# Optimization experiments

Measured on AMD Instinct MI355X. Metric: run time of the kernel, lower is better.

Reference implementation:

```python
import jax, jax.numpy as jnp
import numpy as np

H = 256        # hidden_size
NC = 15        # num_components (decode steps)
V = 26         # vocab_size
E = 64         # embed_dim
B = 65536      # batch


def setup_inputs() -> dict:
    key = jax.random.key(0)
    ks = jax.random.split(key, 8)
    return {
        "context": jax.random.normal(ks[0], (B, H), jnp.float32),
        "embed_table": (jax.random.normal(ks[1], (V, E), jnp.float32) * 0.02),
        "start_embed": (jax.random.normal(ks[2], (E,), jnp.float32) * 0.02),
        "Wp": jax.random.normal(ks[3], (H, H), jnp.float32) / np.sqrt(H),
        "bp": jnp.zeros((H,), jnp.float32),
        "Wi": jax.random.normal(ks[4], (H + E, 4 * H), jnp.float32) / np.sqrt(H + E),
        "Wh": jax.random.normal(ks[5], (H, 4 * H), jnp.float32) / np.sqrt(H),
        "bh": jnp.zeros((4 * H,), jnp.float32),
        "Wo": jax.random.normal(ks[6], (H, V), jnp.float32) / np.sqrt(H),
        "bo": jnp.zeros((V,), jnp.float32),
        "seed": 0,
    }


def _lstm_step(c, h, x, Wi, Wh, bh):
    # flax OptimizedLSTMCell: fused gates, order i, f, g, o; bias on hidden path only
    gates = x @ Wi + h @ Wh + bh            # (B, 4H)
    i, f, g, o = jnp.split(gates, 4, axis=-1)
    c_new = jax.nn.sigmoid(f) * c + jax.nn.sigmoid(i) * jnp.tanh(g)
    h_new = jax.nn.sigmoid(o) * jnp.tanh(c_new)
    return c_new, h_new


def reference(context, embed_table, start_embed, Wp, bp, Wi, Wh, bh, Wo, bo, seed):
    b = context.shape[0]
    h = jnp.tanh(context @ Wp + bp)          # init_proj + tanh
    c = jnp.zeros_like(h)
    prev = jnp.broadcast_to(start_embed, (b, start_embed.shape[0]))
    keys = jax.random.split(jax.random.key(seed), NC)  # one subkey per decode step

    def step(carry, k):
        c, h, prev = carry
        x = jnp.concatenate([context, prev], axis=-1)   # (B, H+E)
        c, h = _lstm_step(c, h, x, Wi, Wh, bh)
        logits = h @ Wo + bo                            # (B, V)
        tok = jax.random.categorical(k, logits, axis=-1)  # (B,) int
        prev = embed_table[tok]                         # embedding lookup
        return (c, h, prev), (logits, tok)

    _, (logits, samples) = jax.lax.scan(step, (c, h, prev), keys)
    # scan stacks on axis 0 (time); move to (B, NC, ...)
    return jnp.transpose(logits, (1, 0, 2)), jnp.transpose(samples, (1, 0))
```

## Files before the change

### kernel.cpp

```cpp
#include <hip/hip_runtime.h>
#include <cstdint>
#include <cstddef>

#define NROWS 8
#define NTHR  256
#define HSZ   256
#define ESZ   64
#define VSZ   26
#define NCOMP 15
#define BATCH 65536

__device__ __forceinline__ uint32_t rotl32(uint32_t v, int d) {
  return (v << d) | (v >> (32 - d));
}

__device__ __forceinline__ void tf2x32(uint32_t kA, uint32_t kB,
                                       uint32_t& x0, uint32_t& x1) {
  uint32_t kC = kA ^ kB ^ 0x1BD11BDAu;
  x0 += kA; x1 += kB;
#define TFR(r) { x0 += x1; x1 = rotl32(x1, r); x1 ^= x0; }
  TFR(13) TFR(15) TFR(26) TFR(6)
  x0 += kB; x1 += kC + 1u;
  TFR(17) TFR(29) TFR(16) TFR(24)
  x0 += kC; x1 += kA + 2u;
  TFR(13) TFR(15) TFR(26) TFR(6)
  x0 += kA; x1 += kB + 3u;
  TFR(17) TFR(29) TFR(16) TFR(24)
  x0 += kB; x1 += kC + 4u;
  TFR(13) TFR(15) TFR(26) TFR(6)
  x0 += kC; x1 += kA + 5u;
#undef TFR
}

__device__ __forceinline__ float xla_tanh(float x) {
  #pragma clang fp contract(off)
  float ax = fabsf(x);
  float xc = fminf(fmaxf(x, -7.90531110763549805f), 7.90531110763549805f);
  float x2 = xc * xc;
  float nu = -2.76076847742355e-16f;
  nu = x2 * nu + 2.00018790482477e-13f;
  nu = x2 * nu + -8.60467152213735e-11f;
  nu = x2 * nu + 5.12229709037114e-08f;
  nu = x2 * nu + 1.48572235717979e-05f;
  nu = x2 * nu + 6.37261928875436e-04f;
  nu = x2 * nu + 4.89352455891786e-03f;
  nu = xc * nu;
  float de = 1.19825839466702e-06f;
  de = x2 * de + 1.18534705686654e-04f;
  de = x2 * de + 2.26843463243900e-03f;
  de = x2 * de + 4.89352518554385e-03f;
  float r = nu / de;
  return (ax < 0.0004f) ? x : r;
}

__device__ __forceinline__ float xla_sigmoid(float x) {
  #pragma clang fp contract(off)
  return 0.5f + 0.5f * xla_tanh(0.5f * x);
}

__device__ __forceinline__ float xla_log(float x) {
  #pragma clang fp contract(off)
  uint32_t bits = __float_as_uint(x);
  int ei = (int)(bits >> 23) - 126;
  float m = __uint_as_float((bits & 0x007FFFFFu) | 0x3F000000u);
  bool lt = m < 0.707106781186547524f;
  float ee = (float)ei - (lt ? 1.0f : 0.0f);
  float mm = (m - 1.0f) + (lt ? m : 0.0f);
  float x2 = mm * mm;
  float x3 = x2 * mm;
  float y  = __builtin_fmaf(7.0376836292E-2f,  mm, -1.1514610310E-1f);
  float y1 = __builtin_fmaf(-1.2420140846E-1f, mm,  1.4249322787E-1f);
  float y2 = __builtin_fmaf(2.0000714765E-1f,  mm, -2.4999993993E-1f);
  y  = __builtin_fmaf(y,  mm, 1.1676998740E-1f);
  y1 = __builtin_fmaf(y1, mm, -1.6668057665E-1f);
  y2 = __builtin_fmaf(y2, mm, 3.3333331174E-1f);
  y  = __builtin_fmaf(y, x3, y1);
  y  = __builtin_fmaf(y, x3, y2);
  y  = y * x3;
  float t1 = ee * -2.12194440e-4f;
  float t2 = 0.5f * x2;
  y  = y + t1;
  mm = mm - t2;
  float t3 = ee * 0.693359375f;
  mm = mm + y;
  mm = mm + t3;
  return mm;
}

template<bool PACKED>
__device__ __forceinline__ void chain8(float* aI, float* aF, float* aG, float* aO,
                                       const float* lds, const float4* W4,
                                       const float* W, int u, int nk) {
  if constexpr (PACKED) {
    const float4* w = W4 + u;
    for (int k = 0; k < nk; ++k) {
      float4 wv = w[(size_t)k * 256];
      float hv[8];
      *(float4*)&hv[0] = *(const float4*)(lds + k * 8);
      *(float4*)&hv[4] = *(const float4*)(lds + k * 8 + 4);
      #pragma unroll
      for (int j = 0; j < 8; ++j) {
        aI[j] = __builtin_fmaf(hv[j], wv.x, aI[j]);
        aF[j] = __builtin_fmaf(hv[j], wv.y, aF[j]);
        aG[j] = __builtin_fmaf(hv[j], wv.z, aG[j]);
        aO[j] = __builtin_fmaf(hv[j], wv.w, aO[j]);
      }
    }
  } else {
    const float* w = W + u;
    for (int k = 0; k < nk; ++k) {
      float wI = w[0], wF = w[256], wG = w[512], wO = w[768];
      w += 1024;
      float hv[8];
      *(float4*)&hv[0] = *(const float4*)(lds + k * 8);
      *(float4*)&hv[4] = *(const float4*)(lds + k * 8 + 4);
      #pragma unroll
      for (int j = 0; j < 8; ++j) {
        aI[j] = __builtin_fmaf(hv[j], wI, aI[j]);
        aF[j] = __builtin_fmaf(hv[j], wF, aF[j]);
        aG[j] = __builtin_fmaf(hv[j], wG, aG[j]);
        aO[j] = __builtin_fmaf(hv[j], wO, aO[j]);
      }
    }
  }
}

__global__ void repack_w(const float* __restrict__ W, float4* __restrict__ W4, int n) {
  int i = blockIdx.x * blockDim.x + threadIdx.x;
  if (i < n) {
    int k = i >> 8, u = i & 255;
    const float* src = W + (size_t)k * 1024 + u;
    W4[i] = make_float4(src[0], src[256], src[512], src[768]);
  }
}

template<bool PACKED>
__global__ __launch_bounds__(NTHR, 4) void belief_main(
    const float* __restrict__ ctx, const float* __restrict__ embed,
    const float* __restrict__ start_e, const float* __restrict__ Wp,
    const float* __restrict__ bp, const float* __restrict__ Wi,
    const float* __restrict__ Wh, const float* __restrict__ bh,
    const float* __restrict__ Wo, const float* __restrict__ bo,
    const int* __restrict__ seedp, float* __restrict__ out,
    const float4* __restrict__ Wi4, const float4* __restrict__ Wh4) {
  __shared__ __align__(16) float hT[HSZ * NROWS];
  __shared__ __align__(16) float ovl[HSZ * NROWS];
  __shared__ float boLds[VSZ];

  float* ctxT   = ovl;
  float* prevT  = ovl;
  float* scores = ovl + ESZ * NROWS;
  int*   tokLds = (int*)(ovl + ESZ * NROWS + NROWS * VSZ);
  uint32_t* skLds = (uint32_t*)(tokLds + NROWS);

  const int t = threadIdx.x;
  const int b0 = blockIdx.x * NROWS;

  #pragma unroll
  for (int r = 0; r < NROWS; ++r)
    ctxT[t * NROWS + r] = ctx[(size_t)(b0 + r) * HSZ + t];
  if (t < VSZ) boLds[t] = bo[t];
  __syncthreads();

  float c[NROWS];
  {
    float acc[NROWS];
    #pragma unroll
    for (int r = 0; r < NROWS; ++r) acc[r] = 0.0f;
    const float* wp = Wp + t;
    for (int m = 0; m < HSZ; ++m) {
      float w = wp[(size_t)m * HSZ];
      float hv[8];
      *(float4*)&hv[0] = *(const float4*)&ctxT[m * NROWS];
      *(float4*)&hv[4] = *(const float4*)&ctxT[m * NROWS + 4];
      #pragma unroll
      for (int j = 0; j < 8; ++j) acc[j] = __builtin_fmaf(hv[j], w, acc[j]);
    }
    float bpv = bp[t];
    #pragma unroll
    for (int r = 0; r < NROWS; ++r) {
      float s = acc[r] + bpv;
      hT[t * NROWS + r] = xla_tanh(s);
      c[r] = 0.0f;
    }
  }

  float pI[NROWS], pF[NROWS], pG[NROWS], pO[NROWS];
  #pragma unroll
  for (int r = 0; r < NROWS; ++r) { pI[r] = 0.f; pF[r] = 0.f; pG[r] = 0.f; pO[r] = 0.f; }
  chain8<PACKED>(pI, pF, pG, pO, ctxT, Wi4, Wi, t, HSZ);
  __syncthreads();

  for (int i = t; i < ESZ * NROWS; i += NTHR) prevT[i] = start_e[i >> 3];
  if (t < NCOMP) {
    uint32_t x0 = 0u, x1 = (uint32_t)t;
    tf2x32(0u, (uint32_t)seedp[0], x0, x1);
    skLds[2 * t] = x0; skLds[2 * t + 1] = x1;
  }
  __syncthreads();

  const float bhI = bh[t], bhF = bh[256 + t], bhG = bh[512 + t], bhO = bh[768 + t];
  const float*  WiP  = Wi  + (size_t)HSZ * 1024;
  const float4* WiP4 = Wi4 + (size_t)HSZ * 256;

  for (int s = 0; s < NCOMP; ++s) {
    float bI[NROWS], bF[NROWS], bG[NROWS], bO[NROWS];
    #pragma unroll
    for (int r = 0; r < NROWS; ++r) { bI[r] = 0.f; bF[r] = 0.f; bG[r] = 0.f; bO[r] = 0.f; }
    chain8<PACKED>(bI, bF, bG, bO, hT, Wh4, Wh, t, HSZ);

    float aI[NROWS], aF[NROWS], aG[NROWS], aO[NROWS];
    #pragma unroll
    for (int r = 0; r < NROWS; ++r) { aI[r] = pI[r]; aF[r] = pF[r]; aG[r] = pG[r]; aO[r] = pO[r]; }
    chain8<PACKED>(aI, aF, aG, aO, prevT, WiP4, WiP, t, ESZ);

    float hnew[NROWS];
    {
      #pragma clang fp contract(off)
      #pragma unroll
      for (int r = 0; r < NROWS; ++r) {
        float gi = (aI[r] + bI[r]) + bhI;
        float gf = (aF[r] + bF[r]) + bhF;
        float gg = (aG[r] + bG[r]) + bhG;
        float go = (aO[r] + bO[r]) + bhO;
        float si = xla_sigmoid(gi);
        float sf = xla_sigmoid(gf);
        float tg = xla_tanh(gg);
        float so = xla_sigmoid(go);
        float cn = sf * c[r] + si * tg;
        c[r] = cn;
        hnew[r] = so * xla_tanh(cn);
      }
    }
    __syncthreads();
    #pragma unroll
    for (int r = 0; r < NROWS; ++r) hT[t * NROWS + r] = hnew[r];
    __syncthreads();

    uint32_t sk0 = skLds[2 * s], sk1 = skLds[2 * s + 1];
    if (t < NROWS * VSZ) {
      int r = t / VSZ, v = t - r * VSZ;
      float acc = 0.0f;
      for (int k = 0; k < HSZ; ++k)
        acc = __builtin_fmaf(hT[k * NROWS + r], Wo[k * VSZ + v], acc);
      float logit = acc + boLds[v];
      out[(size_t)(b0 + r) * (NCOMP * VSZ) + s * VSZ + v] = logit;

      uint32_t n = (uint32_t)(b0 + r) * VSZ + (uint32_t)v;
      uint32_t x0 = 0u, x1 = n;
      tf2x32(sk0, sk1, x0, x1);
      uint32_t rb = x0 ^ x1;
      float f = __uint_as_float((rb >> 9) | 0x3F800000u) - 1.0f;
      float uu;
      {
        #pragma clang fp contract(off)
        uu = f + 1.17549435082228751e-38f;
      }
      uu = fmaxf(1.17549435082228751e-38f, uu);
      float l1 = xla_log(uu);
      float g = -xla_log(-l1);
      {
        #pragma clang fp contract(off)
        scores[r * VSZ + v] = g + logit;
      }
    }
    __syncthreads();

    if (t < NROWS) {
      float mbest = scores[t * VSZ];
      int ibest = 0;
      for (int v = 1; v < VSZ; ++v) {
        float sc = scores[t * VSZ + v];
        if (sc > mbest) { mbest = sc; ibest = v; }
      }
      tokLds[t] = ibest;
      out[(size_t)BATCH * (NCOMP * VSZ) + (size_t)(b0 + t) * NCOMP + s] = (float)ibest;
    }
    __syncthreads();
    if (s < NCOMP - 1) {
      for (int i = t; i < ESZ * NROWS; i += NTHR) {
        int e = i >> 3, r = i & 7;
        prevT[i] = embed[tokLds[r] * ESZ + e];
      }
    }
    __syncthreads();
  }
}

extern "C" void kernel_launch(void* const* d_in, const int* in_sizes, int n_in,
                              void* d_out, int out_size, void* d_ws, size_t ws_size,
                              hipStream_t stream) {
  const float* ctx     = (const float*)d_in[0];
  const float* embed   = (const float*)d_in[1];
  const float* start_e = (const float*)d_in[2];
  const float* Wp      = (const float*)d_in[3];
  const float* bp      = (const float*)d_in[4];
  const float* Wi      = (const float*)d_in[5];
  const float* Wh      = (const float*)d_in[6];
  const float* bh      = (const float*)d_in[7];
  const float* Wo      = (const float*)d_in[8];
  const float* bo      = (const float*)d_in[9];
  const int*   seedp   = (const int*)d_in[10];
  float* out = (float*)d_out;

  size_t wi4_elems = (size_t)(HSZ + ESZ) * 256;
  size_t wh4_elems = (size_t)HSZ * 256;
  size_t need = (wi4_elems + wh4_elems) * sizeof(float4);
  int packed = (d_ws != nullptr && ws_size >= need) ? 1 : 0;
  float4* Wi4 = (float4*)d_ws;
  float4* Wh4 = Wi4 + wi4_elems;

  if (packed) {
    int nWi = (int)wi4_elems, nWh = (int)wh4_elems;
    hipLaunchKernelGGL(repack_w, dim3((nWi + 255) / 256), dim3(256), 0, stream, Wi, Wi4, nWi);
    hipLaunchKernelGGL(repack_w, dim3((nWh + 255) / 256), dim3(256), 0, stream, Wh, Wh4, nWh);
    hipLaunchKernelGGL(belief_main<true>, dim3(BATCH / NROWS), dim3(NTHR), 0, stream,
                       ctx, embed, start_e, Wp, bp, Wi, Wh, bh, Wo, bo, seedp,
                       out, Wi4, Wh4);
  } else {
    hipLaunchKernelGGL(belief_main<false>, dim3(BATCH / NROWS), dim3(NTHR), 0, stream,
                       ctx, embed, start_e, Wp, bp, Wi, Wh, bh, Wo, bo, seedp,
                       out, Wi4, Wh4);
  }
}
```

Before: 12.08 ms.

## Use packed v2f FMAs, spill context gate preactivations to workspace, drop weight repack

The gate matmul chains now use two-wide float vectors so the compiler can emit packed FP32 FMA instructions, and they read the original interleaved weight layout instead of a repacked float4 copy. The repack kernels go away. In the workspace path, the per-row context contribution to the gates (32 values per thread) is written to global memory once and reloaded every step instead of staying live in registers. This frees registers to hold occupancy at 4 waves, at the cost of extra global traffic each step and four scalar weight loads in place of one float4 load.

```diff
diff --git a/kernel.cpp b/kernel.cpp
--- a/kernel.cpp
+++ b/kernel.cpp
@@ -9,6 +9,19 @@
 #define VSZ   26
 #define NCOMP 15
 #define BATCH 65536
+#define NBLK  (BATCH / NROWS)
+#define NTOT  ((size_t)NBLK * NTHR)
+
+typedef float v2f __attribute__((ext_vector_type(2)));
+
+__device__ __forceinline__ v2f vfma(v2f a, v2f b, v2f c) {
+#if __has_builtin(__builtin_elementwise_fma)
+  return __builtin_elementwise_fma(a, b, c);
+#else
+  v2f r; r[0] = __builtin_fmaf(a[0], b[0], c[0]); r[1] = __builtin_fmaf(a[1], b[1], c[1]);
+  return r;
+#endif
+}
 
 __device__ __forceinline__ uint32_t rotl32(uint32_t v, int d) {
   return (v << d) | (v >> (32 - d));
@@ -87,62 +100,38 @@
   return mm;
 }
 
-template<bool PACKED>
-__device__ __forceinline__ void chain8(float* aI, float* aF, float* aG, float* aO,
-                                       const float* lds, const float4* W4,
-                                       const float* W, int u, int nk) {
-  if constexpr (PACKED) {
-    const float4* w = W4 + u;
-    for (int k = 0; k < nk; ++k) {
-      float4 wv = w[(size_t)k * 256];
-      float hv[8];
-      *(float4*)&hv[0] = *(const float4*)(lds + k * 8);
-      *(float4*)&hv[4] = *(const float4*)(lds + k * 8 + 4);
-      #pragma unroll
-      for (int j = 0; j < 8; ++j) {
-        aI[j] = __builtin_fmaf(hv[j], wv.x, aI[j]);
-        aF[j] = __builtin_fmaf(hv[j], wv.y, aF[j]);
-        aG[j] = __builtin_fmaf(hv[j], wv.z, aG[j]);
-        aO[j] = __builtin_fmaf(hv[j], wv.w, aO[j]);
-      }
-    }
-  } else {
-    const float* w = W + u;
-    for (int k = 0; k < nk; ++k) {
-      float wI = w[0], wF = w[256], wG = w[512], wO = w[768];
-      w += 1024;
-      float hv[8];
-      *(float4*)&hv[0] = *(const float4*)(lds + k * 8);
-      *(float4*)&hv[4] = *(const float4*)(lds + k * 8 + 4);
-      #pragma unroll
-      for (int j = 0; j < 8; ++j) {
-        aI[j] = __builtin_fmaf(hv[j], wI, aI[j]);
-        aF[j] = __builtin_fmaf(hv[j], wF, aF[j]);
-        aG[j] = __builtin_fmaf(hv[j], wG, aG[j]);
-        aO[j] = __builtin_fmaf(hv[j], wO, aO[j]);
-      }
-    }
+__device__ __forceinline__ void chainp(v2f aI[4], v2f aF[4], v2f aG[4], v2f aO[4],
+                                       const float* lds, const float* W, int u, int nk) {
+  const float* w = W + u;
+  #pragma unroll 2
+  for (int k = 0; k < nk; ++k) {
+    float wI = w[0], wF = w[256], wG = w[512], wO = w[768];
+    w += 1024;
+    v2f wIv = {wI, wI}, wFv = {wF, wF}, wGv = {wG, wG}, wOv = {wO, wO};
+    v2f h0 = *(const v2f*)(lds + k * 8 + 0);
+    v2f h1 = *(const v2f*)(lds + k * 8 + 2);
+    v2f h2 = *(const v2f*)(lds + k * 8 + 4);
+    v2f h3 = *(const v2f*)(lds + k * 8 + 6);
+    aI[0] = vfma(h0, wIv, aI[0]); aI[1] = vfma(h1, wIv, aI[1]);
+    aI[2] = vfma(h2, wIv, aI[2]); aI[3] = vfma(h3, wIv, aI[3]);
+    aF[0] = vfma(h0, wFv, aF[0]); aF[1] = vfma(h1, wFv, aF[1]);
+    aF[2] = vfma(h2, wFv, aF[2]); aF[3] = vfma(h3, wFv, aF[3]);
+    aG[0] = vfma(h0, wGv, aG[0]); aG[1] = vfma(h1, wGv, aG[1]);
+    aG[2] = vfma(h2, wGv, aG[2]); aG[3] = vfma(h3, wGv, aG[3]);
+    aO[0] = vfma(h0, wOv, aO[0]); aO[1] = vfma(h1, wOv, aO[1]);
+    aO[2] = vfma(h2, wOv, aO[2]); aO[3] = vfma(h3, wOv, aO[3]);
   }
 }
 
-__global__ void repack_w(const float* __restrict__ W, float4* __restrict__ W4, int n) {
-  int i = blockIdx.x * blockDim.x + threadIdx.x;
-  if (i < n) {
-    int k = i >> 8, u = i & 255;
-    const float* src = W + (size_t)k * 1024 + u;
-    W4[i] = make_float4(src[0], src[256], src[512], src[768]);
-  }
-}
-
-template<bool PACKED>
-__global__ __launch_bounds__(NTHR, 4) void belief_main(
+template<bool WSPREF, int MINW>
+__global__ __launch_bounds__(NTHR, MINW) void belief_main(
     const float* __restrict__ ctx, const float* __restrict__ embed,
     const float* __restrict__ start_e, const float* __restrict__ Wp,
     const float* __restrict__ bp, const float* __restrict__ Wi,
     const float* __restrict__ Wh, const float* __restrict__ bh,
     const float* __restrict__ Wo, const float* __restrict__ bo,
     const int* __restrict__ seedp, float* __restrict__ out,
-    const float4* __restrict__ Wi4, const float4* __restrict__ Wh4) {
+    float4* __restrict__ ctxG) {
   __shared__ __align__(16) float hT[HSZ * NROWS];
   __shared__ __align__(16) float ovl[HSZ * NROWS];
   __shared__ float boLds[VSZ];
@@ -155,6 +144,7 @@
 
   const int t = threadIdx.x;
   const int b0 = blockIdx.x * NROWS;
+  const size_t gid = (size_t)blockIdx.x * NTHR + t;
 
   #pragma unroll
   for (int r = 0; r < NROWS; ++r)
@@ -164,126 +154,240 @@
 
   float c[NROWS];
   {
-    float acc[NROWS];
+    v2f acc[4];
     #pragma unroll
-    for (int r = 0; r < NROWS; ++r) acc[r] = 0.0f;
+    for (int q = 0; q < 4; ++q) acc[q] = (v2f){0.f, 0.f};
     const float* wp = Wp + t;
     for (int m = 0; m < HSZ; ++m) {
       float w = wp[(size_t)m * HSZ];
-      float hv[8];
-      *(float4*)&hv[0] = *(const float4*)&ctxT[m * NROWS];
-      *(float4*)&hv[4] = *(const float4*)&ctxT[m * NROWS + 4];
+      v2f wv = {w, w};
       #pragma unroll
-      for (int j = 0; j < 8; ++j) acc[j] = __builtin_fmaf(hv[j], w, acc[j]);
+      for (int q = 0; q < 4; ++q)
+        acc[q] = vfma(*(const v2f*)(ctxT + m * NROWS + 2 * q), wv, acc[q]);
     }
     float bpv = bp[t];
     #pragma unroll
     for (int r = 0; r < NROWS; ++r) {
-      float s = acc[r] + bpv;
+      float s = acc[r >> 1][r & 1] + bpv;
       hT[t * NROWS + r] = xla_tanh(s);
       c[r] = 0.0f;
     }
   }
 
-  float pI[NROWS], pF[NROWS], pG[NROWS], pO[NROWS];
-  #pragma unroll
-  for (int r = 0; r < NROWS; ++r) { pI[r] = 0.f; pF[r] = 0.f; pG[r] = 0.f; pO[r] = 0.f; }
-  chain8<PACKED>(pI, pF, pG, pO, ctxT, Wi4, Wi, t, HSZ);
-  __syncthreads();
-
-  for (int i = t; i < ESZ * NROWS; i += NTHR) prevT[i] = start_e[i >> 3];
-  if (t < NCOMP) {
-    uint32_t x0 = 0u, x1 = (uint32_t)t;
-    tf2x32(0u, (uint32_t)seedp[0], x0, x1);
-    skLds[2 * t] = x0; skLds[2 * t + 1] = x1;
-  }
-  __syncthreads();
-
-  const float bhI = bh[t], bhF = bh[256 + t], bhG = bh[512 + t], bhO = bh[768 + t];
-  const float*  WiP  = Wi  + (size_t)HSZ * 1024;
-  const float4* WiP4 = Wi4 + (size_t)HSZ * 256;
-
-  for (int s = 0; s < NCOMP; ++s) {
-    float bI[NROWS], bF[NROWS], bG[NROWS], bO[NROWS];
+  {
+    v2f pI[4], pF[4], pG[4], pO[4];
     #pragma unroll
-    for (int r = 0; r < NROWS; ++r) { bI[r] = 0.f; bF[r] = 0.f; bG[r] = 0.f; bO[r] = 0.f; }
-    chain8<PACKED>(bI, bF, bG, bO, hT, Wh4, Wh, t, HSZ);
-
-    float aI[NROWS], aF[NROWS], aG[NROWS], aO[NROWS];
-    #pragma unroll
-    for (int r = 0; r < NROWS; ++r) { aI[r] = pI[r]; aF[r] = pF[r]; aG[r] = pG[r]; aO[r] = pO[r]; }
-    chain8<PACKED>(aI, aF, aG, aO, prevT, WiP4, WiP, t, ESZ);
-
-    float hnew[NROWS];
-    {
-      #pragma clang fp contract(off)
+    for (int q = 0; q < 4; ++q) {
+      pI[q] = (v2f){0.f, 0.f}; pF[q] = (v2f){0.f, 0.f};
+      pG[q] = (v2f){0.f, 0.f}; pO[q] = (v2f){0.f, 0.f};
+    }
+    chainp(pI, pF, pG, pO, ctxT, Wi, t, HSZ);
+    if constexpr (WSPREF) {
       #pragma unroll
-      for (int r = 0; r < NROWS; ++r) {
-        float gi = (aI[r] + bI[r]) + bhI;
-        float gf = (aF[r] + bF[r]) + bhF;
-        float gg = (aG[r] + bG[r]) + bhG;
-        float go = (aO[r] + bO[r]) + bhO;
-        float si = xla_sigmoid(gi);
-        float sf = xla_sigmoid(gf);
-        float tg = xla_tanh(gg);
-        float so = xla_sigmoid(go);
-        float cn = sf * c[r] + si * tg;
-        c[r] = cn;
-        hnew[r] = so * xla_tanh(cn);
+      for (int q = 0; q < 4; ++q) {
+        ctxG[(size_t)q * NTOT + gid]       = make_float4(pI[q][0], pI[q][1], pF[q][0], pF[q][1]);
+        ctxG[(size_t)(4 + q) * NTOT + gid] = make_float4(pG[q][0], pG[q][1], pO[q][0], pO[q][1]);
+      }
+      __syncthreads();
+      for (int i = t; i < ESZ * NROWS; i += NTHR) prevT[i] = start_e[i >> 3];
+      if (t < NCOMP) {
+        uint32_t x0 = 0u, x1 = (uint32_t)t;
+        tf2x32(0u, (uint32_t)seedp[0], x0, x1);
+        skLds[2 * t] = x0; skLds[2 * t + 1] = x1;
+      }
+      __syncthreads();
+
+      const float bhI = bh[t], bhF = bh[256 + t], bhG = bh[512 + t], bhO = bh[768 + t];
+      const float* WiP = Wi + (size_t)HSZ * 1024;
+
+      for (int s = 0; s < NCOMP; ++s) {
+        v2f aI[4], aF[4], aG[4], aO[4];
+        #pragma unroll
+        for (int q = 0; q < 4; ++q) {
+          float4 f = ctxG[(size_t)q * NTOT + gid];
+          float4 g = ctxG[(size_t)(4 + q) * NTOT + gid];
+          aI[q] = (v2f){f.x, f.y}; aF[q] = (v2f){f.z, f.w};
+          aG[q] = (v2f){g.x, g.y}; aO[q] = (v2f){g.z, g.w};
+        }
+        chainp(aI, aF, aG, aO, prevT, WiP, t, ESZ);
+
+        v2f bI[4], bF[4], bG[4], bO[4];
+        #pragma unroll
+        for (int q = 0; q < 4; ++q) {
+          bI[q] = (v2f){0.f, 0.f}; bF[q] = (v2f){0.f, 0.f};
+          bG[q] = (v2f){0.f, 0.f}; bO[q] = (v2f){0.f, 0.f};
+        }
+        chainp(bI, bF, bG, bO, hT, Wh, t, HSZ);
+
+        float hnew[NROWS];
+        {
+          #pragma clang fp contract(off)
+          #pragma unroll
+          for (int r = 0; r < NROWS; ++r) {
+            int q = r >> 1, hh = r & 1;
+            float gi = (aI[q][hh] + bI[q][hh]) + bhI;
+            float gf = (aF[q][hh] + bF[q][hh]) + bhF;
+            float gg = (aG[q][hh] + bG[q][hh]) + bhG;
+            float go = (aO[q][hh] + bO[q][hh]) + bhO;
+            float si = xla_sigmoid(gi);
+            float sf = xla_sigmoid(gf);
+            float tg = xla_tanh(gg);
+            float so = xla_sigmoid(go);
+            float cn = sf * c[r] + si * tg;
+            c[r] = cn;
+            hnew[r] = so * xla_tanh(cn);
+          }
+        }
+        __syncthreads();
+        #pragma unroll
+        for (int r = 0; r < NROWS; ++r) hT[t * NROWS + r] = hnew[r];
+        __syncthreads();
+
+        uint32_t sk0 = skLds[2 * s], sk1 = skLds[2 * s + 1];
+        if (t < NROWS * VSZ) {
+          int r = t / VSZ, v = t - r * VSZ;
+          float acc = 0.0f;
+          for (int k = 0; k < HSZ; ++k)
+            acc = __builtin_fmaf(hT[k * NROWS + r], Wo[k * VSZ + v], acc);
+          float logit = acc + boLds[v];
+          out[(size_t)(b0 + r) * (NCOMP * VSZ) + s * VSZ + v] = logit;
+
+          uint32_t n = (uint32_t)(b0 + r) * VSZ + (uint32_t)v;
+          uint32_t x0 = 0u, x1 = n;
+          tf2x32(sk0, sk1, x0, x1);
+          uint32_t rb = x0 ^ x1;
+          float f = __uint_as_float((rb >> 9) | 0x3F800000u) - 1.0f;
+          float uu;
+          {
+            #pragma clang fp contract(off)
+            uu = f + 1.17549435082228751e-38f;
+          }
+          uu = fmaxf(1.17549435082228751e-38f, uu);
+          float l1 = xla_log(uu);
+          float g = -xla_log(-l1);
+          {
+            #pragma clang fp contract(off)
+            scores[r * VSZ + v] = g + logit;
+          }
+        }
+        __syncthreads();
+
+        if (t < NROWS) {
+          float mbest = scores[t * VSZ];
+          int ibest = 0;
+          for (int v = 1; v < VSZ; ++v) {
+            float sc = scores[t * VSZ + v];
+            if (sc > mbest) { mbest = sc; ibest = v; }
+          }
+          tokLds[t] = ibest;
+          out[(size_t)BATCH * (NCOMP * VSZ) + (size_t)(b0 + t) * NCOMP + s] = (float)ibest;
+        }
+        __syncthreads();
+        if (s < NCOMP - 1) {
+          for (int i = t; i < ESZ * NROWS; i += NTHR) {
+            int e = i >> 3, r = i & 7;
+            prevT[i] = embed[tokLds[r] * ESZ + e];
+          }
+        }
+        __syncthreads();
+      }
+    } else {
+      __syncthreads();
+      for (int i = t; i < ESZ * NROWS; i += NTHR) prevT[i] = start_e[i >> 3];
+      if (t < NCOMP) {
+        uint32_t x0 = 0u, x1 = (uint32_t)t;
+        tf2x32(0u, (uint32_t)seedp[0], x0, x1);
+        skLds[2 * t] = x0; skLds[2 * t + 1] = x1;
+      }
+      __syncthreads();
+
+      const float bhI = bh[t], bhF = bh[256 + t], bhG = bh[512 + t], bhO = bh[768 + t];
+      const float* WiP = Wi + (size_t)HSZ * 1024;
+
+      for (int s = 0; s < NCOMP; ++s) {
+        v2f aI[4], aF[4], aG[4], aO[4];
+        #pragma unroll
+        for (int q = 0; q < 4; ++q) { aI[q] = pI[q]; aF[q] = pF[q]; aG[q] = pG[q]; aO[q] = pO[q]; }
+        chainp(aI, aF, aG, aO, prevT, WiP, t, ESZ);
+        v2f bI[4], bF[4], bG[4], bO[4];
+        #pragma unroll
+        for (int q = 0; q < 4; ++q) {
+          bI[q] = (v2f){0.f, 0.f}; bF[q] = (v2f){0.f, 0.f};
+          bG[q] = (v2f){0.f, 0.f}; bO[q] = (v2f){0.f, 0.f};
+        }
+        chainp(bI, bF, bG, bO, hT, Wh, t, HSZ);
+
+        float hnew[NROWS];
+        {
+          #pragma clang fp contract(off)
+          #pragma unroll
+          for (int r = 0; r < NROWS; ++r) {
+            int q = r >> 1, hh = r & 1;
+            float gi = (aI[q][hh] + bI[q][hh]) + bhI;
+            float gf = (aF[q][hh] + bF[q][hh]) + bhF;
+            float gg = (aG[q][hh] + bG[q][hh]) + bhG;
+            float go = (aO[q][hh] + bO[q][hh]) + bhO;
+            float si = xla_sigmoid(gi);
+            float sf = xla_sigmoid(gf);
+            float tg = xla_tanh(gg);
+            float so = xla_sigmoid(go);
+            float cn = sf * c[r] + si * tg;
+            c[r] = cn;
+            hnew[r] = so * xla_tanh(cn);
+          }
+        }
+        __syncthreads();
+        #pragma unroll
+        for (int r = 0; r < NROWS; ++r) hT[t * NROWS + r] = hnew[r];
+        __syncthreads();
+
+        uint32_t sk0 = skLds[2 * s], sk1 = skLds[2 * s + 1];
+        if (t < NROWS * VSZ) {
+          int r = t / VSZ, v = t - r * VSZ;
+          float acc = 0.0f;
+          for (int k = 0; k < HSZ; ++k)
+            acc = __builtin_fmaf(hT[k * NROWS + r], Wo[k * VSZ + v], acc);
+          float logit = acc + boLds[v];
+          out[(size_t)(b0 + r) * (NCOMP * VSZ) + s * VSZ + v] = logit;
+          uint32_t n = (uint32_t)(b0 + r) * VSZ + (uint32_t)v;
+          uint32_t x0 = 0u, x1 = n;
+          tf2x32(sk0, sk1, x0, x1);
+          uint32_t rb = x0 ^ x1;
+          float f = __uint_as_float((rb >> 9) | 0x3F800000u) - 1.0f;
+          float uu;
+          {
+            #pragma clang fp contract(off)
+            uu = f + 1.17549435082228751e-38f;
+          }
+          uu = fmaxf(1.17549435082228751e-38f, uu);
+          float l1 = xla_log(uu);
+          float g = -xla_log(-l1);
+          {
+            #pragma clang fp contract(off)
+            scores[r * VSZ + v] = g + logit;
+          }
+        }
+        __syncthreads();
+        if (t < NROWS) {
+          float mbest = scores[t * VSZ];
+          int ibest = 0;
+          for (int v = 1; v < VSZ; ++v) {
+            float sc = scores[t * VSZ + v];
+            if (sc > mbest) { mbest = sc; ibest = v; }
+          }
+          tokLds[t] = ibest;
+          out[(size_t)BATCH * (NCOMP * VSZ) + (size_t)(b0 + t) * NCOMP + s] = (float)ibest;
+        }
+        __syncthreads();
+        if (s < NCOMP - 1) {
+          for (int i = t; i < ESZ * NROWS; i += NTHR) {
+            int e = i >> 3, r = i & 7;
+            prevT[i] = embed[tokLds[r] * ESZ + e];
+          }
+        }
+        __syncthreads();
       }
     }
-    __syncthreads();
-    #pragma unroll
-    for (int r = 0; r < NROWS; ++r) hT[t * NROWS + r] = hnew[r];
-    __syncthreads();
-
-    uint32_t sk0 = skLds[2 * s], sk1 = skLds[2 * s + 1];
-    if (t < NROWS * VSZ) {
-      int r = t / VSZ, v = t - r * VSZ;
-      float acc = 0.0f;
-      for (int k = 0; k < HSZ; ++k)
-        acc = __builtin_fmaf(hT[k * NROWS + r], Wo[k * VSZ + v], acc);
-      float logit = acc + boLds[v];
-      out[(size_t)(b0 + r) * (NCOMP * VSZ) + s * VSZ + v] = logit;
-
-      uint32_t n = (uint32_t)(b0 + r) * VSZ + (uint32_t)v;
-      uint32_t x0 = 0u, x1 = n;
-      tf2x32(sk0, sk1, x0, x1);
-      uint32_t rb = x0 ^ x1;
-      float f = __uint_as_float((rb >> 9) | 0x3F800000u) - 1.0f;
-      float uu;
-      {
-        #pragma clang fp contract(off)
-        uu = f + 1.17549435082228751e-38f;
-      }
-      uu = fmaxf(1.17549435082228751e-38f, uu);
-      float l1 = xla_log(uu);
-      float g = -xla_log(-l1);
-      {
-        #pragma clang fp contract(off)
-        scores[r * VSZ + v] = g + logit;
-      }
-    }
-    __syncthreads();
-
-    if (t < NROWS) {
-      float mbest = scores[t * VSZ];
-      int ibest = 0;
-      for (int v = 1; v < VSZ; ++v) {
-        float sc = scores[t * VSZ + v];
-        if (sc > mbest) { mbest = sc; ibest = v; }
-      }
-      tokLds[t] = ibest;
-      out[(size_t)BATCH * (NCOMP * VSZ) + (size_t)(b0 + t) * NCOMP + s] = (float)ibest;
-    }
-    __syncthreads();
-    if (s < NCOMP - 1) {
-      for (int i = t; i < ESZ * NROWS; i += NTHR) {
-        int e = i >> 3, r = i & 7;
-        prevT[i] = embed[tokLds[r] * ESZ + e];
-      }
-    }
-    __syncthreads();
   }
 }
 
@@ -303,23 +407,14 @@
   const int*   seedp   = (const int*)d_in[10];
   float* out = (float*)d_out;
 
-  size_t wi4_elems = (size_t)(HSZ + ESZ) * 256;
-  size_t wh4_elems = (size_t)HSZ * 256;
-  size_t need = (wi4_elems + wh4_elems) * sizeof(float4);
-  int packed = (d_ws != nullptr && ws_size >= need) ? 1 : 0;
-  float4* Wi4 = (float4*)d_ws;
-  float4* Wh4 = Wi4 + wi4_elems;
-
-  if (packed) {
-    int nWi = (int)wi4_elems, nWh = (int)wh4_elems;
-    hipLaunchKernelGGL(repack_w, dim3((nWi + 255) / 256), dim3(256), 0, stream, Wi, Wi4, nWi);
-    hipLaunchKernelGGL(repack_w, dim3((nWh + 255) / 256), dim3(256), 0, stream, Wh, Wh4, nWh);
-    hipLaunchKernelGGL(belief_main<true>, dim3(BATCH / NROWS), dim3(NTHR), 0, stream,
-                       ctx, embed, start_e, Wp, bp, Wi, Wh, bh, Wo, bo, seedp,
-                       out, Wi4, Wh4);
+  size_t need = NTOT * 8 * sizeof(float4);
+  float4* ctxG = (float4*)d_ws;
+
+  if (d_ws != nullptr && ws_size >= need) {
+    hipLaunchKernelGGL((belief_main<true, 4>), dim3(NBLK), dim3(NTHR), 0, stream,
+                       ctx, embed, start_e, Wp, bp, Wi, Wh, bh, Wo, bo, seedp, out, ctxG);
   } else {
-    hipLaunchKernelGGL(belief_main<false>, dim3(BATCH / NROWS), dim3(NTHR), 0, stream,
-                       ctx, embed, start_e, Wp, bp, Wi, Wh, bh, Wo, bo, seedp,
-                       out, Wi4, Wh4);
+    hipLaunchKernelGGL((belief_main<false, 3>), dim3(NBLK), dim3(NTHR), 0, stream,
+                       ctx, embed, start_e, Wp, bp, Wi, Wh, bh, Wo, bo, seedp, out, ctxG);
   }
 }
```

Result: no change. 12.22 ms (+1.2%).

## Spill context gate partials to LDS, drop weight repack, relax launch bounds

Applied to the files above, without the earlier changes.

The per-row context contribution to the gates (pI/pF/pG/pO, 32 floats per thread) is now stored in a 32KB shared-memory buffer and reloaded each decode step instead of being held in registers. The float4-packed weight repack kernels and workspace path are removed, so all GEMVs read the strided original weights. Launch bounds go from 4 to 2 blocks per SM, and small unroll pragmas are added to the inner loops. This trades register pressure and the repack launches for more LDS use (about 49KB per block), lower occupancy, and scalar uncoalesced-per-gate weight loads.

```diff
diff --git a/kernel.cpp b/kernel.cpp
--- a/kernel.cpp
+++ b/kernel.cpp
@@ -9,6 +9,7 @@
 #define VSZ   26
 #define NCOMP 15
 #define BATCH 65536
+#define NBLK  (BATCH / NROWS)
 
 __device__ __forceinline__ uint32_t rotl32(uint32_t v, int d) {
   return (v << d) | (v >> (32 - d));
@@ -87,71 +88,42 @@
   return mm;
 }
 
-template<bool PACKED>
 __device__ __forceinline__ void chain8(float* aI, float* aF, float* aG, float* aO,
-                                       const float* lds, const float4* W4,
-                                       const float* W, int u, int nk) {
-  if constexpr (PACKED) {
-    const float4* w = W4 + u;
-    for (int k = 0; k < nk; ++k) {
-      float4 wv = w[(size_t)k * 256];
-      float hv[8];
-      *(float4*)&hv[0] = *(const float4*)(lds + k * 8);
-      *(float4*)&hv[4] = *(const float4*)(lds + k * 8 + 4);
-      #pragma unroll
-      for (int j = 0; j < 8; ++j) {
-        aI[j] = __builtin_fmaf(hv[j], wv.x, aI[j]);
-        aF[j] = __builtin_fmaf(hv[j], wv.y, aF[j]);
-        aG[j] = __builtin_fmaf(hv[j], wv.z, aG[j]);
-        aO[j] = __builtin_fmaf(hv[j], wv.w, aO[j]);
-      }
-    }
-  } else {
-    const float* w = W + u;
-    for (int k = 0; k < nk; ++k) {
-      float wI = w[0], wF = w[256], wG = w[512], wO = w[768];
-      w += 1024;
-      float hv[8];
-      *(float4*)&hv[0] = *(const float4*)(lds + k * 8);
-      *(float4*)&hv[4] = *(const float4*)(lds + k * 8 + 4);
-      #pragma unroll
-      for (int j = 0; j < 8; ++j) {
-        aI[j] = __builtin_fmaf(hv[j], wI, aI[j]);
-        aF[j] = __builtin_fmaf(hv[j], wF, aF[j]);
-        aG[j] = __builtin_fmaf(hv[j], wG, aG[j]);
-        aO[j] = __builtin_fmaf(hv[j], wO, aO[j]);
-      }
-    }
-  }
-}
-
-__global__ void repack_w(const float* __restrict__ W, float4* __restrict__ W4, int n) {
-  int i = blockIdx.x * blockDim.x + threadIdx.x;
-  if (i < n) {
-    int k = i >> 8, u = i & 255;
-    const float* src = W + (size_t)k * 1024 + u;
-    W4[i] = make_float4(src[0], src[256], src[512], src[768]);
-  }
-}
-
-template<bool PACKED>
-__global__ __launch_bounds__(NTHR, 4) void belief_main(
+                                       const float* lds, const float* W, int u, int nk) {
+  const float* w = W + u;
+  #pragma unroll 2
+  for (int k = 0; k < nk; ++k) {
+    float wI = w[0], wF = w[256], wG = w[512], wO = w[768];
+    w += 1024;
+    float hv[8];
+    *(float4*)&hv[0] = *(const float4*)(lds + k * 8);
+    *(float4*)&hv[4] = *(const float4*)(lds + k * 8 + 4);
+    #pragma unroll
+    for (int j = 0; j < 8; ++j) {
+      aI[j] = __builtin_fmaf(hv[j], wI, aI[j]);
+      aF[j] = __builtin_fmaf(hv[j], wF, aF[j]);
+      aG[j] = __builtin_fmaf(hv[j], wG, aG[j]);
+      aO[j] = __builtin_fmaf(hv[j], wO, aO[j]);
+    }
+  }
+}
+
+__global__ __launch_bounds__(NTHR, 2) void belief_main(
     const float* __restrict__ ctx, const float* __restrict__ embed,
     const float* __restrict__ start_e, const float* __restrict__ Wp,
     const float* __restrict__ bp, const float* __restrict__ Wi,
     const float* __restrict__ Wh, const float* __restrict__ bh,
     const float* __restrict__ Wo, const float* __restrict__ bo,
-    const int* __restrict__ seedp, float* __restrict__ out,
-    const float4* __restrict__ Wi4, const float4* __restrict__ Wh4) {
+    const int* __restrict__ seedp, float* __restrict__ out) {
+  __shared__ __align__(16) float G0[NROWS * 1024];
   __shared__ __align__(16) float hT[HSZ * NROWS];
-  __shared__ __align__(16) float ovl[HSZ * NROWS];
+  __shared__ __align__(16) float prevT[ESZ * NROWS];
+  __shared__ float scores[NROWS * VSZ];
   __shared__ float boLds[VSZ];
-
-  float* ctxT   = ovl;
-  float* prevT  = ovl;
-  float* scores = ovl + ESZ * NROWS;
-  int*   tokLds = (int*)(ovl + ESZ * NROWS + NROWS * VSZ);
-  uint32_t* skLds = (uint32_t*)(tokLds + NROWS);
+  __shared__ int tokLds[NROWS];
+  __shared__ uint32_t skLds[NCOMP * 2];
+
+  float* ctxT = G0;
 
   const int t = threadIdx.x;
   const int b0 = blockIdx.x * NROWS;
@@ -168,6 +140,7 @@
     #pragma unroll
     for (int r = 0; r < NROWS; ++r) acc[r] = 0.0f;
     const float* wp = Wp + t;
+    #pragma unroll 2
     for (int m = 0; m < HSZ; ++m) {
       float w = wp[(size_t)m * HSZ];
       float hv[8];
@@ -185,12 +158,20 @@
     }
   }
 
-  float pI[NROWS], pF[NROWS], pG[NROWS], pO[NROWS];
-  #pragma unroll
-  for (int r = 0; r < NROWS; ++r) { pI[r] = 0.f; pF[r] = 0.f; pG[r] = 0.f; pO[r] = 0.f; }
-  chain8<PACKED>(pI, pF, pG, pO, ctxT, Wi4, Wi, t, HSZ);
-  __syncthreads();
-
+  {
+    float pI[NROWS], pF[NROWS], pG[NROWS], pO[NROWS];
+    #pragma unroll
+    for (int r = 0; r < NROWS; ++r) { pI[r] = 0.f; pF[r] = 0.f; pG[r] = 0.f; pO[r] = 0.f; }
+    chain8(pI, pF, pG, pO, ctxT, Wi, t, HSZ);
+    __syncthreads();
+    #pragma unroll
+    for (int r = 0; r < NROWS; ++r) {
+      G0[r * 1024 + t]       = pI[r];
+      G0[r * 1024 + 256 + t] = pF[r];
+      G0[r * 1024 + 512 + t] = pG[r];
+      G0[r * 1024 + 768 + t] = pO[r];
+    }
+  }
   for (int i = t; i < ESZ * NROWS; i += NTHR) prevT[i] = start_e[i >> 3];
   if (t < NCOMP) {
     uint32_t x0 = 0u, x1 = (uint32_t)t;
@@ -200,19 +181,23 @@
   __syncthreads();
 
   const float bhI = bh[t], bhF = bh[256 + t], bhG = bh[512 + t], bhO = bh[768 + t];
-  const float*  WiP  = Wi  + (size_t)HSZ * 1024;
-  const float4* WiP4 = Wi4 + (size_t)HSZ * 256;
+  const float* WiP = Wi + (size_t)HSZ * 1024;
 
   for (int s = 0; s < NCOMP; ++s) {
     float bI[NROWS], bF[NROWS], bG[NROWS], bO[NROWS];
     #pragma unroll
     for (int r = 0; r < NROWS; ++r) { bI[r] = 0.f; bF[r] = 0.f; bG[r] = 0.f; bO[r] = 0.f; }
-    chain8<PACKED>(bI, bF, bG, bO, hT, Wh4, Wh, t, HSZ);
+    chain8(bI, bF, bG, bO, hT, Wh, t, HSZ);
 
     float aI[NROWS], aF[NROWS], aG[NROWS], aO[NROWS];
     #pragma unroll
-    for (int r = 0; r < NROWS; ++r) { aI[r] = pI[r]; aF[r] = pF[r]; aG[r] = pG[r]; aO[r] = pO[r]; }
-    chain8<PACKED>(aI, aF, aG, aO, prevT, WiP4, WiP, t, ESZ);
+    for (int r = 0; r < NROWS; ++r) {
+      aI[r] = G0[r * 1024 + t];
+      aF[r] = G0[r * 1024 + 256 + t];
+      aG[r] = G0[r * 1024 + 512 + t];
+      aO[r] = G0[r * 1024 + 768 + t];
+    }
+    chain8(aI, aF, aG, aO, prevT, WiP, t, ESZ);
 
     float hnew[NROWS];
     {
@@ -241,6 +226,7 @@
     if (t < NROWS * VSZ) {
       int r = t / VSZ, v = t - r * VSZ;
       float acc = 0.0f;
+      #pragma unroll 4
       for (int k = 0; k < HSZ; ++k)
         acc = __builtin_fmaf(hT[k * NROWS + r], Wo[k * VSZ + v], acc);
       float logit = acc + boLds[v];
@@ -303,23 +289,6 @@
   const int*   seedp   = (const int*)d_in[10];
   float* out = (float*)d_out;
 
-  size_t wi4_elems = (size_t)(HSZ + ESZ) * 256;
-  size_t wh4_elems = (size_t)HSZ * 256;
-  size_t need = (wi4_elems + wh4_elems) * sizeof(float4);
-  int packed = (d_ws != nullptr && ws_size >= need) ? 1 : 0;
-  float4* Wi4 = (float4*)d_ws;
-  float4* Wh4 = Wi4 + wi4_elems;
-
-  if (packed) {
-    int nWi = (int)wi4_elems, nWh = (int)wh4_elems;
-    hipLaunchKernelGGL(repack_w, dim3((nWi + 255) / 256), dim3(256), 0, stream, Wi, Wi4, nWi);
-    hipLaunchKernelGGL(repack_w, dim3((nWh + 255) / 256), dim3(256), 0, stream, Wh, Wh4, nWh);
-    hipLaunchKernelGGL(belief_main<true>, dim3(BATCH / NROWS), dim3(NTHR), 0, stream,
-                       ctx, embed, start_e, Wp, bp, Wi, Wh, bh, Wo, bo, seedp,
-                       out, Wi4, Wh4);
-  } else {
-    hipLaunchKernelGGL(belief_main<false>, dim3(BATCH / NROWS), dim3(NTHR), 0, stream,
-                       ctx, embed, start_e, Wp, bp, Wi, Wh, bh, Wo, bo, seedp,
-                       out, Wi4, Wh4);
-  }
-}
+  hipLaunchKernelGGL(belief_main, dim3(NBLK), dim3(NTHR), 0, stream,
+                     ctx, embed, start_e, Wp, bp, Wi, Wh, bh, Wo, bo, seedp, out);
+}
```

Measured after the change: 11.27 ms. -6.7%, faster.
